# Kernel optimization log

Measured on AMD Instinct MI355X. Metric: run time of the kernel, lower is better.

Reference implementation:

```python
import jax, jax.numpy as jnp
import numpy as np

KH, KW = 3, 3
STRIDE = (1, 1)


def setup_inputs() -> dict:
    key = jax.random.key(0)
    k1, k2, k3 = jax.random.split(key, 3)
    N, C, H, W = 16, 128, 64, 64
    O = 128
    x = jax.random.normal(k1, (N, C, H, W), dtype=jnp.float32)
    # Flat weight layout [O, C*KH*KW], matching torch reshape of [O,C,KH,KW]
    weight = jax.random.normal(k2, (O, C * KH * KW), dtype=jnp.float32) * 0.02
    bias = jax.random.normal(k3, (O, 1), dtype=jnp.float32) * 0.02
    return {"x": x, "weight": weight, "bias": bias}


def reference(x, weight, bias):
    O = weight.shape[0]
    C = x.shape[1]
    # [O, C*KH*KW] -> [O, C, KH, KW]; flattening order (C major, then kh, kw)
    # matches the module's unfold/permute im2col layout.
    w4 = weight.reshape(O, C, KH, KW)
    out = jax.lax.conv_general_dilated(
        x, w4,
        window_strides=STRIDE,
        padding='VALID',
        dimension_numbers=('NCHW', 'OIHW', 'NCHW'),
    )
    return out + bias.reshape(1, O, 1, 1)
```

## Files before the change

kernel.cpp:

```cpp
#include <hip/hip_runtime.h>
#include <stdint.h>

#define AS_G __attribute__((address_space(1)))
#define AS_L __attribute__((address_space(3)))

typedef __bf16 bf16x8 __attribute__((ext_vector_type(8)));
typedef float  f32x4  __attribute__((ext_vector_type(4)));

static constexpr int NIMG = 16, CIN = 128, H = 64, W = 64, OCH = 128;
static constexpr int HO = 62, WO = 62;
static constexpr int PIX = HO * WO;
static constexpr int M_TOT = NIMG * PIX;
static constexpr int K_TOT = CIN * 9;
static constexpr int BM = 128;
static constexpr int NCHUNK = 9;
static constexpr int GRID = (M_TOT + BM - 1) / BM;

__device__ __forceinline__ unsigned short f2bf(float f) {
    union { float f; uint32_t u; } v; v.f = f;
    uint32_t u = v.u;
    return (unsigned short)((u + 0x7FFFu + ((u >> 16) & 1u)) >> 16);
}

__global__ __launch_bounds__(256) void prep_kernel(const float* __restrict__ x,
                                                   const float* __restrict__ wsrc,
                                                   unsigned short* __restrict__ xt,
                                                   unsigned short* __restrict__ bpd) {
    __shared__ float lds[CIN][W + 4];
    if (blockIdx.x < NIMG * H) {
        const int n   = blockIdx.x >> 6;
        const int h   = blockIdx.x & 63;
        const int tid = threadIdx.x;
        {
            const int c  = tid >> 1;
            const int w0 = (tid & 1) * 32;
            const float* src = x + (((size_t)(n * CIN + c) * H + h) * W + w0);
            #pragma unroll
            for (int j = 0; j < 8; ++j) {
                float4 v = *reinterpret_cast<const float4*>(src + j * 4);
                *reinterpret_cast<float4*>(&lds[c][w0 + j * 4]) = v;
            }
        }
        __syncthreads();
        {
            const int w  = tid >> 2;
            const int c0 = (tid & 3) * 32;
            unsigned short* dst = xt + (((size_t)(n * H + h) * W + w) * CIN + c0);
            uint32_t pk[16];
            #pragma unroll
            for (int j = 0; j < 16; ++j) {
                uint32_t lo = f2bf(lds[c0 + 2 * j][w]);
                uint32_t hi = f2bf(lds[c0 + 2 * j + 1][w]);
                pk[j] = lo | (hi << 16);
            }
            #pragma unroll
            for (int j = 0; j < 4; ++j) {
                *reinterpret_cast<uint4*>(dst + j * 8) =
                    make_uint4(pk[4 * j], pk[4 * j + 1], pk[4 * j + 2], pk[4 * j + 3]);
            }
        }
    } else {
        int tid = (blockIdx.x - NIMG * H) * 256 + threadIdx.x;
        if (tid < OCH * K_TOT) {
            int o  = tid / K_TOT;
            int kp = tid - o * K_TOT;
            int t  = kp >> 7;
            int c  = kp & 127;
            bpd[tid] = f2bf(wsrc[o * K_TOT + c * 9 + t]);
        }
    }
}

__global__ __launch_bounds__(256) void gemm_kernel(const unsigned short* __restrict__ xt,
                                                   const unsigned short* __restrict__ bp,
                                                   const float* __restrict__ bias,
                                                   float* __restrict__ out) {
    __shared__ alignas(16) char lds[2 * 32768];
    const int tid  = threadIdx.x;
    const int wv   = tid >> 6;
    const int lane = tid & 63;
    const int lr   = lane & 15, lq = lane >> 4;
    const int m0   = blockIdx.x * BM;

    int bOff[8];
    #pragma unroll
    for (int p = 0; p < 8; ++p) {
        int s = (wv * 8 + p) * 64 + lane;
        int o = s >> 4, q = s & 15;
        bOff[p] = o * K_TOT + ((q ^ (o & 7)) * 8);
    }
    auto stageB = [&](int buf, int t) {
        const unsigned short* src = bp + t * 128;
        char* dst = lds + buf * 32768;
        #pragma unroll
        for (int p = 0; p < 8; ++p)
            __builtin_amdgcn_global_load_lds(
                (AS_G unsigned int*)(src + bOff[p]),
                (AS_L unsigned int*)(dst + (wv * 8 + p) * 1024), 16, 0, 0);
    };

    int base0[2], ybase[2];
    bool valid[2];
    #pragma unroll
    for (int mi = 0; mi < 2; ++mi) {
        int m = m0 + wv * 32 + mi * 16 + lr;
        valid[mi] = (m < M_TOT);
        if (m >= M_TOT) m = M_TOT - 1;
        int n  = m / PIX;
        int r  = m - n * PIX;
        int y  = r / WO;
        int xx = r - y * WO;
        base0[mi] = ((n * H + y) * W + xx) * CIN + lq * 8;
        ybase[mi] = n * OCH * PIX + y * WO + xx;
    }

    f32x4 acc[2][8];
    #pragma unroll
    for (int a = 0; a < 2; ++a)
        #pragma unroll
        for (int b = 0; b < 8; ++b)
            acc[a][b] = (f32x4){0.f, 0.f, 0.f, 0.f};

    stageB(0, 0);
    __syncthreads();

    const int wxor = (lr & 7) << 4;
    for (int t = 0; t < NCHUNK; ++t) {
        if (t + 1 < NCHUNK) stageB((t & 1) ^ 1, t + 1);
        const char* wb = lds + (t & 1) * 32768;
        const int kh = t / 3, kw = t - kh * 3;
        const int tapoff = (kh * W + kw) * CIN;
        #pragma unroll
        for (int ks = 0; ks < 4; ++ks) {
            bf16x8 af[2], wf[8];
            #pragma unroll
            for (int mi = 0; mi < 2; ++mi)
                af[mi] = *(const bf16x8*)(xt + base0[mi] + tapoff + ks * 32);
            const int colw = (ks * 64 + lq * 16) ^ wxor;
            #pragma unroll
            for (int ni = 0; ni < 8; ++ni)
                wf[ni] = *(const bf16x8*)(wb + ni * 4096 + lr * 256 + colw);
            #pragma unroll
            for (int mi = 0; mi < 2; ++mi)
                #pragma unroll
                for (int ni = 0; ni < 8; ++ni)
                    acc[mi][ni] = __builtin_amdgcn_mfma_f32_16x16x32_bf16(
                        wf[ni], af[mi], acc[mi][ni], 0, 0, 0);
        }
        __syncthreads();
    }

    #pragma unroll
    for (int mi = 0; mi < 2; ++mi) {
        if (valid[mi]) {
            float* ob = out + ybase[mi];
            #pragma unroll
            for (int ni = 0; ni < 8; ++ni) {
                f32x4 bv = *(const f32x4*)(bias + ni * 16 + lq * 4);
                #pragma unroll
                for (int j = 0; j < 4; ++j)
                    ob[(size_t)(ni * 16 + lq * 4 + j) * PIX] = acc[mi][ni][j] + bv[j];
            }
        }
    }
}

extern "C" void kernel_launch(void* const* d_in, const int* in_sizes, int n_in,
                              void* d_out, int out_size, void* d_ws, size_t ws_size,
                              hipStream_t stream) {
    const float* x    = (const float*)d_in[0];
    const float* wsrc = (const float*)d_in[1];
    const float* bias = (const float*)d_in[2];
    float* out = (float*)d_out;
    unsigned short* xt = (unsigned short*)d_ws;
    unsigned short* bp = xt + (size_t)NIMG * H * W * CIN;
    prep_kernel<<<dim3(NIMG * H + (OCH * K_TOT + 255) / 256), dim3(256), 0, stream>>>(
        x, wsrc, xt, bp);
    gemm_kernel<<<dim3(GRID), dim3(256), 0, stream>>>(xt, bp, bias, out);
}
```

Baseline: 47.36 us.

## Hold half of the weights in LDS and use 512-pixel tiles with XCD-aware block mapping

The GEMM block now preloads one half of the output channels' full K-dimension weights (64x1152 bf16, 144 KB) into LDS once, instead of double-buffering per-tap weight chunks with a barrier per tap. Each block computes 512 pixels by 64 channels, with each wave holding 8x4 accumulators, and the grid is twice the number of M blocks. Block IDs are remapped so the two channel halves of a pixel tile run on the same XCD, which is meant to share activation reads through L2. The trade-off is one block per CU because of the large LDS footprint, more register pressure, and activation data loaded twice across the two channel halves.

```diff
diff --git a/kernel.cpp b/kernel.cpp
--- a/kernel.cpp
+++ b/kernel.cpp
@@ -12,9 +12,10 @@
 static constexpr int PIX = HO * WO;
 static constexpr int M_TOT = NIMG * PIX;
 static constexpr int K_TOT = CIN * 9;
-static constexpr int BM = 128;
-static constexpr int NCHUNK = 9;
-static constexpr int GRID = (M_TOT + BM - 1) / BM;
+static constexpr int MBLK = 512;
+static constexpr int NMB = (M_TOT + MBLK - 1) / MBLK;
+static constexpr int NWG = NMB * 2;
+static constexpr int LDS_BYTES = 64 * K_TOT * 2;
 
 __device__ __forceinline__ unsigned short f2bf(float f) {
     union { float f; uint32_t u; } v; v.f = f;
@@ -71,95 +72,117 @@
     }
 }
 
-__global__ __launch_bounds__(256) void gemm_kernel(const unsigned short* __restrict__ xt,
-                                                   const unsigned short* __restrict__ bp,
-                                                   const float* __restrict__ bias,
-                                                   float* __restrict__ out) {
-    __shared__ alignas(16) char lds[2 * 32768];
+__global__ __launch_bounds__(256, 1) void gemm_kernel(const unsigned short* __restrict__ xt,
+                                                      const unsigned short* __restrict__ bp,
+                                                      const float* __restrict__ bias,
+                                                      float* __restrict__ out) {
+    extern __shared__ char lds[];
     const int tid  = threadIdx.x;
     const int wv   = tid >> 6;
     const int lane = tid & 63;
     const int lr   = lane & 15, lq = lane >> 4;
-    const int m0   = blockIdx.x * BM;
-
-    int bOff[8];
-    #pragma unroll
-    for (int p = 0; p < 8; ++p) {
-        int s = (wv * 8 + p) * 64 + lane;
-        int o = s >> 4, q = s & 15;
-        bOff[p] = o * K_TOT + ((q ^ (o & 7)) * 8);
-    }
-    auto stageB = [&](int buf, int t) {
-        const unsigned short* src = bp + t * 128;
-        char* dst = lds + buf * 32768;
-        #pragma unroll
-        for (int p = 0; p < 8; ++p)
+
+    const int orig = blockIdx.x;
+    const int xcd  = orig & 7;
+    const int idx  = orig >> 3;
+    const int wg   = (xcd < 2 ? xcd * 31 : 62 + (xcd - 2) * 30) + idx;
+    const int mblk = wg >> 1;
+    const int oh   = wg & 1;
+
+    {
+        const unsigned short* wbase = bp + oh * 64 * K_TOT;
+        #pragma unroll
+        for (int p = 0; p < 36; ++p) {
+            int s  = p * 256 + tid;
+            int o  = s / 144;
+            int q  = s - o * 144;
+            int Lx = (q * 16) ^ ((o & 7) << 4);
             __builtin_amdgcn_global_load_lds(
-                (AS_G unsigned int*)(src + bOff[p]),
-                (AS_L unsigned int*)(dst + (wv * 8 + p) * 1024), 16, 0, 0);
-    };
-
-    int base0[2], ybase[2];
-    bool valid[2];
-    #pragma unroll
-    for (int mi = 0; mi < 2; ++mi) {
-        int m = m0 + wv * 32 + mi * 16 + lr;
+                (AS_G unsigned int*)(wbase + o * K_TOT + (Lx >> 1)),
+                (AS_L unsigned int*)(lds + p * 4096 + wv * 1024),
+                16, 0, 0);
+        }
+    }
+
+    int pixBase[8], obase[8];
+    bool valid[8];
+    #pragma unroll
+    for (int mi = 0; mi < 8; ++mi) {
+        int m = mblk * MBLK + wv * 128 + mi * 16 + lr;
         valid[mi] = (m < M_TOT);
         if (m >= M_TOT) m = M_TOT - 1;
         int n  = m / PIX;
         int r  = m - n * PIX;
         int y  = r / WO;
         int xx = r - y * WO;
-        base0[mi] = ((n * H + y) * W + xx) * CIN + lq * 8;
-        ybase[mi] = n * OCH * PIX + y * WO + xx;
-    }
-
-    f32x4 acc[2][8];
-    #pragma unroll
-    for (int a = 0; a < 2; ++a)
-        #pragma unroll
-        for (int b = 0; b < 8; ++b)
+        pixBase[mi] = ((n * H + y) * W + xx) * CIN;
+        obase[mi]   = n * OCH * PIX + y * WO + xx;
+    }
+
+    int bOff[4][4];
+    #pragma unroll
+    for (int ks = 0; ks < 4; ++ks)
+        #pragma unroll
+        for (int ni = 0; ni < 4; ++ni)
+            bOff[ks][ni] = (ni * 16 + lr) * 2304 +
+                           ((ks * 64 + lq * 16) ^ ((lr & 7) << 4));
+
+    f32x4 acc[8][4];
+    #pragma unroll
+    for (int a = 0; a < 8; ++a)
+        #pragma unroll
+        for (int b = 0; b < 4; ++b)
             acc[a][b] = (f32x4){0.f, 0.f, 0.f, 0.f};
 
-    stageB(0, 0);
-    __syncthreads();
-
-    const int wxor = (lr & 7) << 4;
-    for (int t = 0; t < NCHUNK; ++t) {
-        if (t + 1 < NCHUNK) stageB((t & 1) ^ 1, t + 1);
-        const char* wb = lds + (t & 1) * 32768;
+    asm volatile("s_waitcnt vmcnt(0)" ::: "memory");
+    __builtin_amdgcn_s_barrier();
+
+    for (int t = 0; t < 9; ++t) {
         const int kh = t / 3, kw = t - kh * 3;
         const int tapoff = (kh * W + kw) * CIN;
-        #pragma unroll
-        for (int ks = 0; ks < 4; ++ks) {
-            bf16x8 af[2], wf[8];
-            #pragma unroll
-            for (int mi = 0; mi < 2; ++mi)
-                af[mi] = *(const bf16x8*)(xt + base0[mi] + tapoff + ks * 32);
-            const int colw = (ks * 64 + lq * 16) ^ wxor;
-            #pragma unroll
-            for (int ni = 0; ni < 8; ++ni)
-                wf[ni] = *(const bf16x8*)(wb + ni * 4096 + lr * 256 + colw);
-            #pragma unroll
-            for (int mi = 0; mi < 2; ++mi)
+        const int kfrag  = lq * 8;
+        const int tlds   = t * 256;
+
+        bf16x8 bfr[4][4];
+        #pragma unroll
+        for (int ks = 0; ks < 4; ++ks)
+            #pragma unroll
+            for (int ni = 0; ni < 4; ++ni)
+                bfr[ks][ni] = *(const bf16x8*)(lds + tlds + bOff[ks][ni]);
+
+        bf16x8 af[8][4];
+        #pragma unroll
+        for (int mi = 0; mi < 8; ++mi) {
+            const unsigned short* ap = xt + pixBase[mi] + tapoff + kfrag;
+            #pragma unroll
+            for (int ks = 0; ks < 4; ++ks)
+                af[mi][ks] = *(const bf16x8*)(ap + ks * 32);
+        }
+
+        #pragma unroll
+        for (int mi = 0; mi < 8; ++mi)
+            #pragma unroll
+            for (int ks = 0; ks < 4; ++ks)
                 #pragma unroll
-                for (int ni = 0; ni < 8; ++ni)
+                for (int ni = 0; ni < 4; ++ni)
                     acc[mi][ni] = __builtin_amdgcn_mfma_f32_16x16x32_bf16(
-                        wf[ni], af[mi], acc[mi][ni], 0, 0, 0);
-        }
-        __syncthreads();
-    }
-
-    #pragma unroll
-    for (int mi = 0; mi < 2; ++mi) {
+                        bfr[ks][ni], af[mi][ks], acc[mi][ni], 0, 0, 0);
+    }
+
+    f32x4 bv[4];
+    #pragma unroll
+    for (int ni = 0; ni < 4; ++ni)
+        bv[ni] = *(const f32x4*)(bias + oh * 64 + ni * 16 + lq * 4);
+    #pragma unroll
+    for (int mi = 0; mi < 8; ++mi) {
         if (valid[mi]) {
-            float* ob = out + ybase[mi];
-            #pragma unroll
-            for (int ni = 0; ni < 8; ++ni) {
-                f32x4 bv = *(const f32x4*)(bias + ni * 16 + lq * 4);
+            float* ob = out + obase[mi];
+            #pragma unroll
+            for (int ni = 0; ni < 4; ++ni) {
+                const int o = oh * 64 + ni * 16 + lq * 4;
                 #pragma unroll
                 for (int j = 0; j < 4; ++j)
-                    ob[(size_t)(ni * 16 + lq * 4 + j) * PIX] = acc[mi][ni][j] + bv[j];
+                    ob[(size_t)(o + j) * PIX] = acc[mi][ni][j] + bv[ni][j];
             }
         }
     }
@@ -176,5 +199,5 @@
     unsigned short* bp = xt + (size_t)NIMG * H * W * CIN;
     prep_kernel<<<dim3(NIMG * H + (OCH * K_TOT + 255) / 256), dim3(256), 0, stream>>>(
         x, wsrc, xt, bp);
-    gemm_kernel<<<dim3(GRID), dim3(256), 0, stream>>>(xt, bp, bias, out);
-}
+    gemm_kernel<<<dim3(NWG), dim3(256), LDS_BYTES, stream>>>(xt, bp, bias, out);
+}
```

Result: slower. 78.46 us (+65.7%).
